# Kernel tuning notes

Hardware: AMD Instinct MI355X
Metric: run time of the kernel (lower is better)

Reference implementation:

```python
import jax, jax.numpy as jnp
import numpy as np

N = 100_000      # target ('paper') nodes
E_RAND = 500_000 # random metapath edges (self-loops added on top)
C = 256          # channels
H = 8            # heads
D = C // H       # proj_dim = 32
SEM = 128        # semantic attention hidden
NEG_SLOPE = 0.2


def _edges(k):
    e = jax.random.randint(k, (2, E_RAND), 0, N, dtype=jnp.int32)
    loops = jnp.broadcast_to(jnp.arange(N, dtype=jnp.int32), (2, N))
    return jnp.concatenate([e, loops], axis=1)  # [2, E_RAND + N]


def setup_inputs() -> dict:
    key = jax.random.key(0)
    ks = jax.random.split(key, 9)
    return {
        "x": jax.random.normal(ks[0], (N, C), dtype=jnp.float32),
        "W": jax.random.normal(ks[1], (D, C), dtype=jnp.float32) * (1.0 / np.sqrt(C)),
        "att1": jax.random.normal(ks[2], (H, 2 * D), dtype=jnp.float32) * (1.0 / np.sqrt(2 * D)),
        "att2": jax.random.normal(ks[3], (H, 2 * D), dtype=jnp.float32) * (1.0 / np.sqrt(2 * D)),
        "fc_w": jax.random.normal(ks[4], (SEM, C), dtype=jnp.float32) * (1.0 / np.sqrt(C)),
        "fc_b": jnp.zeros((SEM,), dtype=jnp.float32),
        "q": jax.random.normal(ks[5], (SEM,), dtype=jnp.float32) * (1.0 / np.sqrt(SEM)),
        "ei1": _edges(ks[6]),
        "ei2": _edges(ks[7]),
    }


def _segment_softmax(e, dst, num_nodes):
    # numerically stable softmax over edges grouped by destination node
    m = jax.ops.segment_max(e, dst, num_segments=num_nodes)      # [N, H]
    ex = jnp.exp(e - m[dst])                                     # [E, H]
    s = jax.ops.segment_sum(ex, dst, num_segments=num_nodes)     # [N, H]
    return ex / s[dst]


def _gat_layer(h, ei, att):
    # h: [N, d] projected target features; ei: [2, E]; att: [H, 2d]
    src, dst = ei[0], ei[1]
    n, d = h.shape
    a_dst, a_src = att[:, :d], att[:, d:]   # cat order in torch: [h_i(dst), h_j(src)]
    # per-edge attention logits [E, H] without materializing [E, H, 2d]
    e = jax.nn.leaky_relu(h[dst] @ a_dst.T + h[src] @ a_src.T, NEG_SLOPE)
    alpha = _segment_softmax(e, dst, n)                          # [E, H]
    m = h[src][:, None, :] * alpha[:, :, None]                   # [E, H, d]
    out = jax.ops.segment_sum(m, dst, num_segments=n)            # [N, H, d]
    return jax.nn.elu(out).reshape(n, H * d)                     # [N, H*d]


def reference(x, W, att1, att2, fc_w, fc_b, q, ei1, ei2):
    # type-specific projection (bias-free Linear): [N, C] -> [N, d]
    h = x @ W.T
    Z1 = _gat_layer(h, ei1, att1)
    Z2 = _gat_layer(h, ei2, att2)
    # semantic attention across meta-paths
    def score(Z):
        return (jnp.tanh(Z @ fc_w.T + fc_b) @ q).mean()
    V = jax.nn.softmax(jnp.stack([score(Z1), score(Z2)]))        # [2]
    return V[0] * Z1 + V[1] * Z2                                 # [N, C]
```

## Files before the change

kernel.cpp:

```cpp
#include <hip/hip_runtime.h>
#include <math.h>

#define Nn 100000
#define Cc 256
#define Dd 32
#define Hh 8
#define SEMk 128
#define PAD 32
#define NEG 0.2f
#define NB1 25000
#define NBS 1563

#if __has_builtin(__builtin_amdgcn_exp2f)
#define EXP2(x) __builtin_amdgcn_exp2f(x)
#else
#define EXP2(x) exp2f(x)
#endif
#define LOG2E 1.44269504088896f

typedef __attribute__((ext_vector_type(8))) short bf16x8;
typedef __attribute__((ext_vector_type(4))) short s16x4;
typedef __attribute__((ext_vector_type(4))) float f32x4;

__device__ __forceinline__ short f2bf(float f) {
    unsigned u = __float_as_uint(f);
    u = (u + 0x7FFF + ((u >> 16) & 1)) >> 16;
    return (short)u;
}

__global__ __launch_bounds__(256) void k_prep(const float* __restrict__ W,
                                              float* __restrict__ Wt,
                                              const float* __restrict__ fcw,
                                              short* __restrict__ fcwb) {
    int i = blockIdx.x * 256 + threadIdx.x;
    if (i < Dd * Cc) {
        int j = i >> 5, k = i & 31;
        Wt[i] = W[k * Cc + j];
    }
    if (i < SEMk * Cc) fcwb[i] = f2bf(fcw[i]);
}

__global__ __launch_bounds__(256) void k_hproj(const float* __restrict__ x,
                                               const float* __restrict__ Wt,
                                               const float* __restrict__ att1,
                                               const float* __restrict__ att2,
                                               float* __restrict__ h,
                                               float* __restrict__ sd1, float* __restrict__ ss1,
                                               float* __restrict__ sd2, float* __restrict__ ss2) {
    __shared__ float4 xs[32 * 65];
    __shared__ float  wt[256 * 36];
    __shared__ float4 hs[32 * 9];
    __shared__ float  a1[8 * 68];
    __shared__ float  a2[8 * 68];

    int t = threadIdx.x;
    int nb = blockIdx.x * 32;

    const float4* xg = (const float4*)x + (size_t)nb * 64;
#pragma unroll
    for (int it = 0; it < 8; ++it) {
        int i = t + it * 256;
        xs[(i >> 6) * 65 + (i & 63)] = xg[i];
    }
    const float4* wg = (const float4*)Wt;
#pragma unroll
    for (int it = 0; it < 8; ++it) {
        int i = t + it * 256;
        *(float4*)&wt[(i >> 3) * 36 + (i & 7) * 4] = wg[i];
    }
#pragma unroll
    for (int it = 0; it < 2; ++it) {
        int i = t + it * 256;
        a1[(i >> 6) * 68 + (i & 63)] = att1[i];
        a2[(i >> 6) * 68 + (i & 63)] = att2[i];
    }
    __syncthreads();

    int nl = t >> 3;
    int dq = t & 7;
    float4 acc = make_float4(0.f, 0.f, 0.f, 0.f);
    const float4* xr = &xs[nl * 65];
#pragma unroll 4
    for (int j4 = 0; j4 < 64; ++j4) {
        float4 xv = xr[j4];
        float4 w0 = *(const float4*)&wt[(j4 * 4 + 0) * 36 + dq * 4];
        float4 w1 = *(const float4*)&wt[(j4 * 4 + 1) * 36 + dq * 4];
        float4 w2 = *(const float4*)&wt[(j4 * 4 + 2) * 36 + dq * 4];
        float4 w3 = *(const float4*)&wt[(j4 * 4 + 3) * 36 + dq * 4];
        acc.x += xv.x * w0.x + xv.y * w1.x + xv.z * w2.x + xv.w * w3.x;
        acc.y += xv.x * w0.y + xv.y * w1.y + xv.z * w2.y + xv.w * w3.y;
        acc.z += xv.x * w0.z + xv.y * w1.z + xv.z * w2.z + xv.w * w3.z;
        acc.w += xv.x * w0.w + xv.y * w1.w + xv.z * w2.w + xv.w * w3.w;
    }
    ((float4*)h)[(size_t)(nb + nl) * 8 + dq] = acc;
    hs[nl * 9 + dq] = acc;
    __syncthreads();

    int nl2 = t >> 3;
    int hh = t & 7;
    float d1 = 0.f, s1 = 0.f, d2 = 0.f, s2 = 0.f;
#pragma unroll
    for (int d4 = 0; d4 < 8; ++d4) {
        float4 hv = hs[nl2 * 9 + d4];
        float4 ad1 = *(const float4*)&a1[hh * 68 + d4 * 4];
        float4 as1 = *(const float4*)&a1[hh * 68 + 32 + d4 * 4];
        float4 ad2 = *(const float4*)&a2[hh * 68 + d4 * 4];
        float4 as2 = *(const float4*)&a2[hh * 68 + 32 + d4 * 4];
        d1 += hv.x * ad1.x + hv.y * ad1.y + hv.z * ad1.z + hv.w * ad1.w;
        s1 += hv.x * as1.x + hv.y * as1.y + hv.z * as1.z + hv.w * as1.w;
        d2 += hv.x * ad2.x + hv.y * ad2.y + hv.z * ad2.z + hv.w * ad2.w;
        s2 += hv.x * as2.x + hv.y * as2.y + hv.z * as2.z + hv.w * as2.w;
    }
    int n = nb + nl2;
    sd1[n * 8 + hh] = d1 * LOG2E; ss1[n * 8 + hh] = s1 * LOG2E;
    sd2[n * 8 + hh] = d2 * LOG2E; ss2[n * 8 + hh] = s2 * LOG2E;
}

__global__ __launch_bounds__(256) void k_scatter(const int* __restrict__ ei1, int E1,
                                                 const int* __restrict__ ei2, int E2,
                                                 int* __restrict__ cnt,
                                                 int* __restrict__ slt1,
                                                 int* __restrict__ slt2) {
    int id = blockIdx.x * 256 + threadIdx.x;
    const int* ei; int e, EE; int* c; int* sl;
    if (id < E1) { ei = ei1; e = id; EE = E1; c = cnt; sl = slt1; }
    else {
        e = id - E1;
        if (e >= E2) return;
        ei = ei2; EE = E2; c = cnt + Nn; sl = slt2;
    }
    int s = ei[e];
    int d = ei[EE + e];
    int pos = atomicAdd(&c[d], 1);
    if (pos < PAD) sl[d * PAD + pos] = s;
}

#define LOADC(S0,S1,S2,S3,A0,A1,A2,A3,V0,V1,V2,V3,BB) do {                         \
    S0 = __shfl(sval, (BB) + 0); S1 = __shfl(sval, (BB) + 1);                      \
    S2 = __shfl(sval, (BB) + 2); S3 = __shfl(sval, (BB) + 3);                      \
    S1 = ((BB) + 1 < deg) ? S1 : n;                                                \
    S2 = ((BB) + 2 < deg) ? S2 : n;                                                \
    S3 = ((BB) + 3 < deg) ? S3 : n;                                                \
    A0 = ssrc[(unsigned)S0 * 8u + hh]; A1 = ssrc[(unsigned)S1 * 8u + hh];          \
    A2 = ssrc[(unsigned)S2 * 8u + hh]; A3 = ssrc[(unsigned)S3 * 8u + hh];          \
    V0 = h4[(unsigned)S0 * 8u + sub];  V1 = h4[(unsigned)S1 * 8u + sub];           \
    V2 = h4[(unsigned)S2 * 8u + sub];  V3 = h4[(unsigned)S3 * 8u + sub];           \
} while (0)

#define CONS(A0,A1,A2,A3,V0,V1,V2,V3,BB) do {                                      \
    float ev_, w_;                                                                 \
    ev_ = sd + A0; ev_ = ev_ > 0.f ? ev_ : NEG * ev_; w_ = EXP2(ev_);              \
    acc.x += w_ * V0.x; acc.y += w_ * V0.y; acc.z += w_ * V0.z; acc.w += w_ * V0.w; ssum += w_; \
    ev_ = sd + A1; ev_ = ev_ > 0.f ? ev_ : NEG * ev_; w_ = EXP2(ev_);              \
    w_ = ((BB) + 1 < deg) ? w_ : 0.f;                                              \
    acc.x += w_ * V1.x; acc.y += w_ * V1.y; acc.z += w_ * V1.z; acc.w += w_ * V1.w; ssum += w_; \
    ev_ = sd + A2; ev_ = ev_ > 0.f ? ev_ : NEG * ev_; w_ = EXP2(ev_);              \
    w_ = ((BB) + 2 < deg) ? w_ : 0.f;                                              \
    acc.x += w_ * V2.x; acc.y += w_ * V2.y; acc.z += w_ * V2.z; acc.w += w_ * V2.w; ssum += w_; \
    ev_ = sd + A3; ev_ = ev_ > 0.f ? ev_ : NEG * ev_; w_ = EXP2(ev_);              \
    w_ = ((BB) + 3 < deg) ? w_ : 0.f;                                              \
    acc.x += w_ * V3.x; acc.y += w_ * V3.y; acc.z += w_ * V3.z; acc.w += w_ * V3.w; ssum += w_; \
} while (0)

__global__ __launch_bounds__(256, 4) void k_gat(const float* __restrict__ h,
                                                const float* __restrict__ sd1, const float* __restrict__ ss1,
                                                const float* __restrict__ sd2, const float* __restrict__ ss2,
                                                const int* __restrict__ cnt,
                                                const int* __restrict__ slt1, const int* __restrict__ slt2,
                                                float* __restrict__ Z1, float* __restrict__ Z2) {
    int blk = blockIdx.x;
    const float* sdst = sd1; const float* ssrc = ss1;
    const int* cc = cnt; const int* sl = slt1; float* Z = Z1;
    if (blk >= NB1) { blk -= NB1; sdst = sd2; ssrc = ss2; cc = cnt + Nn; sl = slt2; Z = Z2; }
    int t = threadIdx.x;
    int lane = t & 63;
    int n = blk * 4 + (t >> 6);
    int deg = cc[n]; if (deg > PAD) deg = PAD;
    int hh = lane >> 3;
    int sub = lane & 7;
    float sd = sdst[n * 8 + hh];
    int sval = sl[n * PAD + (lane & 31)];
    const float4* h4 = (const float4*)h;

    float ssum = 0.f;
    float4 acc = make_float4(0.f, 0.f, 0.f, 0.f);

    int as0, as1, as2, as3;  float aa0, aa1, aa2, aa3;  float4 av0, av1, av2, av3;
    int bs0, bs1, bs2, bs3;  float ba0, ba1, ba2, ba3;  float4 bv0, bv1, bv2, bv3;

    LOADC(as0, as1, as2, as3, aa0, aa1, aa2, aa3, av0, av1, av2, av3, 0);
    int base = 0;
    for (;;) {
        int nxt = base + 4;
        bool more = nxt < deg;
        if (more) LOADC(bs0, bs1, bs2, bs3, ba0, ba1, ba2, ba3, bv0, bv1, bv2, bv3, nxt);
        CONS(aa0, aa1, aa2, aa3, av0, av1, av2, av3, base);
        if (!more) break;
        base = nxt;
        nxt = base + 4;
        more = nxt < deg;
        if (more) LOADC(as0, as1, as2, as3, aa0, aa1, aa2, aa3, av0, av1, av2, av3, nxt);
        CONS(ba0, ba1, ba2, ba3, bv0, bv1, bv2, bv3, base);
        if (!more) break;
        base = nxt;
    }

    float inv = 1.f / ssum;
    float4 o;
    o.x = acc.x * inv; o.y = acc.y * inv; o.z = acc.z * inv; o.w = acc.w * inv;
    o.x = o.x > 0.f ? o.x : __expf(o.x) - 1.f;
    o.y = o.y > 0.f ? o.y : __expf(o.y) - 1.f;
    o.z = o.z > 0.f ? o.z : __expf(o.z) - 1.f;
    o.w = o.w > 0.f ? o.w : __expf(o.w) - 1.f;
    ((float4*)Z)[(size_t)n * 64 + lane] = o;
}

__device__ __forceinline__ float fast_tanh(float x) {
    return 1.f - 2.f / (1.f + __expf(2.f * x));
}

__global__ __launch_bounds__(256) void k_score(const float* __restrict__ Z1,
                        const float* __restrict__ Z2,
                        const short* __restrict__ fcwb,
                        const float* __restrict__ fcb,
                        const float* __restrict__ q,
                        float* __restrict__ Sacc) {
    int blk = blockIdx.x;
    const float* Z = Z1; float* bins = Sacc;
    if (blk >= NBS) { blk -= NBS; Z = Z2; bins = Sacc + 256; }
    int t = threadIdx.x;
    int lane = t & 63;
    int wid = t >> 6;
    int nodebase = blk * 64 + wid * 16;
    if (nodebase >= Nn) return;
    int col = lane & 15;
    int quad = lane >> 4;

    const float* zp = Z + (size_t)(nodebase + col) * Cc + quad * 8;
    bf16x8 af[8];
#pragma unroll
    for (int ks = 0; ks < 8; ++ks) {
        float4 f0 = *(const float4*)(zp + ks * 32);
        float4 f1 = *(const float4*)(zp + ks * 32 + 4);
        bf16x8 a;
        a[0] = f2bf(f0.x); a[1] = f2bf(f0.y); a[2] = f2bf(f0.z); a[3] = f2bf(f0.w);
        a[4] = f2bf(f1.x); a[5] = f2bf(f1.y); a[6] = f2bf(f1.z); a[7] = f2bf(f1.w);
        af[ks] = a;
    }

    f32x4 acc[8];
#pragma unroll
    for (int tt = 0; tt < 8; ++tt) { acc[tt][0] = 0.f; acc[tt][1] = 0.f; acc[tt][2] = 0.f; acc[tt][3] = 0.f; }

    const short* brow = fcwb + (size_t)col * Cc + quad * 8;
#pragma unroll
    for (int ks = 0; ks < 8; ++ks) {
#pragma unroll
        for (int tt = 0; tt < 8; ++tt) {
            bf16x8 b = *(const bf16x8*)(brow + tt * 4096 + ks * 32);
            acc[tt] = __builtin_amdgcn_mfma_f32_16x16x32_bf16(af[ks], b, acc[tt], 0, 0, 0);
        }
    }

    float local = 0.f;
#pragma unroll
    for (int tt = 0; tt < 8; ++tt) {
        int sem = tt * 16 + col;
        float b = fcb[sem], qq = q[sem];
#pragma unroll
        for (int r = 0; r < 4; ++r) local += fast_tanh(acc[tt][r] + b) * qq;
    }
#pragma unroll
    for (int off = 32; off > 0; off >>= 1) local += __shfl_down(local, off);
    if (lane == 0) atomicAdd(&bins[(blk & 15) * 16], local);
}

__global__ __launch_bounds__(256) void k_combine(float* __restrict__ out,
                                                 const float* __restrict__ Z2,
                                                 const float* __restrict__ S) {
    float s1 = 0.f, s2 = 0.f;
#pragma unroll
    for (int i = 0; i < 16; ++i) { s1 += S[i * 16]; s2 += S[256 + i * 16]; }
    s1 *= (1.f / (float)Nn);
    s2 *= (1.f / (float)Nn);
    float mx = fmaxf(s1, s2);
    float e1 = __expf(s1 - mx), e2 = __expf(s2 - mx);
    float inv = 1.f / (e1 + e2);
    float V0 = e1 * inv, V1 = e2 * inv;
    size_t i = (size_t)blockIdx.x * 256 + threadIdx.x;
    if (i < (size_t)Nn * 64) {
        float4 a = ((float4*)out)[i];
        float4 b = ((const float4*)Z2)[i];
        a.x = V0 * a.x + V1 * b.x;
        a.y = V0 * a.y + V1 * b.y;
        a.z = V0 * a.z + V1 * b.z;
        a.w = V0 * a.w + V1 * b.w;
        ((float4*)out)[i] = a;
    }
}

extern "C" void kernel_launch(void* const* d_in, const int* in_sizes, int n_in,
                              void* d_out, int out_size, void* d_ws, size_t ws_size,
                              hipStream_t stream) {
    const float* x    = (const float*)d_in[0];
    const float* W    = (const float*)d_in[1];
    const float* att1 = (const float*)d_in[2];
    const float* att2 = (const float*)d_in[3];
    const float* fcw  = (const float*)d_in[4];
    const float* fcb  = (const float*)d_in[5];
    const float* q    = (const float*)d_in[6];
    const int*   ei1  = (const int*)d_in[7];
    const int*   ei2  = (const int*)d_in[8];
    int E1 = in_sizes[7] / 2;
    int E2 = in_sizes[8] / 2;
    float* out = (float*)d_out;

    char* ws = (char*)d_ws;
    size_t off = 0;
    auto alloc = [&](size_t bytes) -> char* {
        char* p = ws + off;
        off = (off + bytes + 255) & ~(size_t)255;
        return p;
    };
    float* Z2   = (float*)alloc((size_t)Nn * Cc * 4);
    float* h    = (float*)alloc((size_t)Nn * Dd * 4);
    float* sd1  = (float*)alloc((size_t)Nn * Hh * 4);
    float* ss1  = (float*)alloc((size_t)Nn * Hh * 4);
    float* sd2  = (float*)alloc((size_t)Nn * Hh * 4);
    float* ss2  = (float*)alloc((size_t)Nn * Hh * 4);
    int*   cnt  = (int*)alloc((size_t)2 * Nn * 4);
    float* red  = (float*)alloc(2048);
    float* Wt   = (float*)alloc((size_t)Dd * Cc * 4);
    short* fcwb = (short*)alloc((size_t)SEMk * Cc * 2);
    int*   slt1 = (int*)alloc((size_t)Nn * PAD * 4);
    int*   slt2 = (int*)alloc((size_t)Nn * PAD * 4);
    (void)ws_size; (void)n_in; (void)out_size;

    hipMemsetAsync(cnt, 0, (size_t)2 * Nn * 4, stream);
    hipMemsetAsync(red, 0, 2048, stream);

    k_prep<<<(SEMk * Cc + 255) / 256, 256, 0, stream>>>(W, Wt, fcw, fcwb);
    k_hproj<<<Nn / 32, 256, 0, stream>>>(x, Wt, att1, att2, h, sd1, ss1, sd2, ss2);
    k_scatter<<<(E1 + E2 + 255) / 256, 256, 0, stream>>>(ei1, E1, ei2, E2, cnt, slt1, slt2);
    k_gat<<<2 * NB1, 256, 0, stream>>>(h, sd1, ss1, sd2, ss2, cnt, slt1, slt2, out, Z2);
    k_score<<<2 * NBS, 256, 0, stream>>>(out, Z2, fcwb, fcb, q, red);
    k_combine<<<(Nn * 64) / 256, 256, 0, stream>>>(out, Z2, red);
}
```

Before: 543.4 us.

## Fuse semantic-attention scoring into GAT aggregation kernel via shared-memory bf16 tile

The separate score kernel is merged into the GAT kernel. Each 1024-thread block now aggregates 16 nodes, converts the outputs to bf16 in LDS, and then 8 waves each run one 16-column MFMA slice of the fc projection, followed by tanh·q and an atomic add. This removes the re-read of Z1/Z2 from global memory and one kernel launch. In exchange it adds a block-wide barrier, leaves half the waves idle during the scoring phase, and the larger blocks may lower occupancy for the latency-bound gather.

Result: no change. 542.5 us (-0.2%).

```diff
diff --git a/kernel.cpp b/kernel.cpp
--- a/kernel.cpp
+++ b/kernel.cpp
@@ -8,8 +8,7 @@
 #define SEMk 128
 #define PAD 32
 #define NEG 0.2f
-#define NB1 25000
-#define NBS 1563
+#define NBF 6250
 
 #if __has_builtin(__builtin_amdgcn_exp2f)
 #define EXP2(x) __builtin_amdgcn_exp2f(x)
@@ -162,19 +161,26 @@
     acc.x += w_ * V3.x; acc.y += w_ * V3.y; acc.z += w_ * V3.z; acc.w += w_ * V3.w; ssum += w_; \
 } while (0)
 
-__global__ __launch_bounds__(256, 4) void k_gat(const float* __restrict__ h,
-                                                const float* __restrict__ sd1, const float* __restrict__ ss1,
-                                                const float* __restrict__ sd2, const float* __restrict__ ss2,
-                                                const int* __restrict__ cnt,
-                                                const int* __restrict__ slt1, const int* __restrict__ slt2,
-                                                float* __restrict__ Z1, float* __restrict__ Z2) {
+__global__ __launch_bounds__(1024, 8) void k_gatsc(const float* __restrict__ h,
+                                                   const float* __restrict__ sd1, const float* __restrict__ ss1,
+                                                   const float* __restrict__ sd2, const float* __restrict__ ss2,
+                                                   const int* __restrict__ cnt,
+                                                   const int* __restrict__ slt1, const int* __restrict__ slt2,
+                                                   float* __restrict__ Z1, float* __restrict__ Z2,
+                                                   const short* __restrict__ fcwb,
+                                                   const float* __restrict__ fcb,
+                                                   const float* __restrict__ q,
+                                                   float* __restrict__ Sacc) {
+    __shared__ short zls[16 * 264];
     int blk = blockIdx.x;
     const float* sdst = sd1; const float* ssrc = ss1;
     const int* cc = cnt; const int* sl = slt1; float* Z = Z1;
-    if (blk >= NB1) { blk -= NB1; sdst = sd2; ssrc = ss2; cc = cnt + Nn; sl = slt2; Z = Z2; }
+    float* bins = Sacc;
+    if (blk >= NBF) { blk -= NBF; sdst = sd2; ssrc = ss2; cc = cnt + Nn; sl = slt2; Z = Z2; bins = Sacc + 256; }
     int t = threadIdx.x;
     int lane = t & 63;
-    int n = blk * 4 + (t >> 6);
+    int wid = t >> 6;
+    int n = blk * 16 + wid;
     int deg = cc[n]; if (deg > PAD) deg = PAD;
     int hh = lane >> 3;
     int sub = lane & 7;
@@ -213,66 +219,36 @@
     o.z = o.z > 0.f ? o.z : __expf(o.z) - 1.f;
     o.w = o.w > 0.f ? o.w : __expf(o.w) - 1.f;
     ((float4*)Z)[(size_t)n * 64 + lane] = o;
-}
-
-__device__ __forceinline__ float fast_tanh(float x) {
-    return 1.f - 2.f / (1.f + __expf(2.f * x));
-}
-
-__global__ __launch_bounds__(256) void k_score(const float* __restrict__ Z1,
-                        const float* __restrict__ Z2,
-                        const short* __restrict__ fcwb,
-                        const float* __restrict__ fcb,
-                        const float* __restrict__ q,
-                        float* __restrict__ Sacc) {
-    int blk = blockIdx.x;
-    const float* Z = Z1; float* bins = Sacc;
-    if (blk >= NBS) { blk -= NBS; Z = Z2; bins = Sacc + 256; }
-    int t = threadIdx.x;
-    int lane = t & 63;
-    int wid = t >> 6;
-    int nodebase = blk * 64 + wid * 16;
-    if (nodebase >= Nn) return;
+
+    s16x4 b4;
+    b4[0] = f2bf(o.x); b4[1] = f2bf(o.y); b4[2] = f2bf(o.z); b4[3] = f2bf(o.w);
+    *(s16x4*)&zls[wid * 264 + lane * 4] = b4;
+    __syncthreads();
+
+    if (wid >= 8) return;
+
     int col = lane & 15;
     int quad = lane >> 4;
-
-    const float* zp = Z + (size_t)(nodebase + col) * Cc + quad * 8;
-    bf16x8 af[8];
+    const short* zrow = &zls[col * 264 + quad * 8];
+    const short* brow = fcwb + (size_t)(wid * 16 + col) * Cc + quad * 8;
+    f32x4 sacc;
+    sacc[0] = 0.f; sacc[1] = 0.f; sacc[2] = 0.f; sacc[3] = 0.f;
 #pragma unroll
     for (int ks = 0; ks < 8; ++ks) {
-        float4 f0 = *(const float4*)(zp + ks * 32);
-        float4 f1 = *(const float4*)(zp + ks * 32 + 4);
-        bf16x8 a;
-        a[0] = f2bf(f0.x); a[1] = f2bf(f0.y); a[2] = f2bf(f0.z); a[3] = f2bf(f0.w);
-        a[4] = f2bf(f1.x); a[5] = f2bf(f1.y); a[6] = f2bf(f1.z); a[7] = f2bf(f1.w);
-        af[ks] = a;
-    }
-
-    f32x4 acc[8];
-#pragma unroll
-    for (int tt = 0; tt < 8; ++tt) { acc[tt][0] = 0.f; acc[tt][1] = 0.f; acc[tt][2] = 0.f; acc[tt][3] = 0.f; }
-
-    const short* brow = fcwb + (size_t)col * Cc + quad * 8;
-#pragma unroll
-    for (int ks = 0; ks < 8; ++ks) {
-#pragma unroll
-        for (int tt = 0; tt < 8; ++tt) {
-            bf16x8 b = *(const bf16x8*)(brow + tt * 4096 + ks * 32);
-            acc[tt] = __builtin_amdgcn_mfma_f32_16x16x32_bf16(af[ks], b, acc[tt], 0, 0, 0);
-        }
-    }
-
+        bf16x8 a = *(const bf16x8*)(zrow + ks * 32);
+        bf16x8 b = *(const bf16x8*)(brow + ks * 32);
+        sacc = __builtin_amdgcn_mfma_f32_16x16x32_bf16(a, b, sacc, 0, 0, 0);
+    }
     float local = 0.f;
-#pragma unroll
-    for (int tt = 0; tt < 8; ++tt) {
-        int sem = tt * 16 + col;
-        float b = fcb[sem], qq = q[sem];
-#pragma unroll
-        for (int r = 0; r < 4; ++r) local += fast_tanh(acc[tt][r] + b) * qq;
+    {
+        int sem = wid * 16 + col;
+        float bb = fcb[sem], qq = q[sem];
+#pragma unroll
+        for (int r = 0; r < 4; ++r) local += (1.f - 2.f / (1.f + __expf(2.f * (sacc[r] + bb)))) * qq;
     }
 #pragma unroll
     for (int off = 32; off > 0; off >>= 1) local += __shfl_down(local, off);
-    if (lane == 0) atomicAdd(&bins[(blk & 15) * 16], local);
+    if (lane == 0) atomicAdd(&bins[(blk & 31) * 8], local);
 }
 
 __global__ __launch_bounds__(256) void k_combine(float* __restrict__ out,
@@ -280,7 +256,7 @@
                                                  const float* __restrict__ S) {
     float s1 = 0.f, s2 = 0.f;
 #pragma unroll
-    for (int i = 0; i < 16; ++i) { s1 += S[i * 16]; s2 += S[256 + i * 16]; }
+    for (int i = 0; i < 32; ++i) { s1 += S[i * 8]; s2 += S[256 + i * 8]; }
     s1 *= (1.f / (float)Nn);
     s2 *= (1.f / (float)Nn);
     float mx = fmaxf(s1, s2);
@@ -342,7 +318,7 @@
     k_prep<<<(SEMk * Cc + 255) / 256, 256, 0, stream>>>(W, Wt, fcw, fcwb);
     k_hproj<<<Nn / 32, 256, 0, stream>>>(x, Wt, att1, att2, h, sd1, ss1, sd2, ss2);
     k_scatter<<<(E1 + E2 + 255) / 256, 256, 0, stream>>>(ei1, E1, ei2, E2, cnt, slt1, slt2);
-    k_gat<<<2 * NB1, 256, 0, stream>>>(h, sd1, ss1, sd2, ss2, cnt, slt1, slt2, out, Z2);
-    k_score<<<2 * NBS, 256, 0, stream>>>(out, Z2, fcwb, fcb, q, red);
+    k_gatsc<<<2 * NBF, 1024, 0, stream>>>(h, sd1, ss1, sd2, ss2, cnt, slt1, slt2,
+                                          out, Z2, fcwb, fcb, q, red);
     k_combine<<<(Nn * 64) / 256, 256, 0, stream>>>(out, Z2, red);
 }
```

## Stage score-kernel Z tiles through LDS with coalesced swizzled direct loads

Applied to the files above, without the earlier changes.

The semantic score kernel now loads each wave's 16x256 Z tile into shared memory with global_load_lds in coalesced 1KB row chunks, using an XOR swizzle to avoid bank conflicts. Fragments are then read from LDS instead of through strided per-lane global loads. Each wave handles one 16-node task, and the B-operand loads are batched ahead of the MFMAs. The atomic bins are spread over 32 slots. The cost is 64KB of LDS per block, which limits occupancy.

Result: faster. 528.8 us (-2.7%).

```diff
diff --git a/kernel.cpp b/kernel.cpp
--- a/kernel.cpp
+++ b/kernel.cpp
@@ -9,7 +9,7 @@
 #define PAD 32
 #define NEG 0.2f
 #define NB1 25000
-#define NBS 1563
+#define NTASK 12500
 
 #if __has_builtin(__builtin_amdgcn_exp2f)
 #define EXP2(x) __builtin_amdgcn_exp2f(x)
@@ -219,29 +219,47 @@
     return 1.f - 2.f / (1.f + __expf(2.f * x));
 }
 
+#define SWZ(off, r) ((off) ^ (((r) & 7) << 4))
+
 __global__ __launch_bounds__(256) void k_score(const float* __restrict__ Z1,
                         const float* __restrict__ Z2,
                         const short* __restrict__ fcwb,
                         const float* __restrict__ fcb,
                         const float* __restrict__ q,
                         float* __restrict__ Sacc) {
-    int blk = blockIdx.x;
-    const float* Z = Z1; float* bins = Sacc;
-    if (blk >= NBS) { blk -= NBS; Z = Z2; bins = Sacc + 256; }
+    __shared__ float zst[4 * 4096];
     int t = threadIdx.x;
     int lane = t & 63;
     int wid = t >> 6;
-    int nodebase = blk * 64 + wid * 16;
-    if (nodebase >= Nn) return;
+    int task = blockIdx.x * 4 + wid;
+    const float* Z = Z1; float* bins = Sacc;
+    int tile = task;
+    if (task >= NTASK / 2) { Z = Z2; bins = Sacc + 256; tile = task - NTASK / 2; }
+    int nodebase = tile * 16;
+    float* myst = &zst[wid * 4096];
+
+    const char* zb = (const char*)(Z + (size_t)nodebase * Cc);
+#pragma unroll
+    for (int r = 0; r < 16; ++r) {
+        const char* src = zb + r * 1024 + SWZ(lane * 16, r);
+        __builtin_amdgcn_global_load_lds(
+            (const __attribute__((address_space(1))) void*)src,
+            (__attribute__((address_space(3))) void*)(myst + r * 256),
+            16, 0, 0);
+    }
+    asm volatile("s_waitcnt vmcnt(0)" ::: "memory");
+    __builtin_amdgcn_sched_barrier(0);
+
     int col = lane & 15;
     int quad = lane >> 4;
 
-    const float* zp = Z + (size_t)(nodebase + col) * Cc + quad * 8;
+    const char* rowp = (const char*)myst + col * 1024;
     bf16x8 af[8];
 #pragma unroll
     for (int ks = 0; ks < 8; ++ks) {
-        float4 f0 = *(const float4*)(zp + ks * 32);
-        float4 f1 = *(const float4*)(zp + ks * 32 + 4);
+        int b0 = ks * 128 + quad * 32;
+        float4 f0 = *(const float4*)(rowp + SWZ(b0, col));
+        float4 f1 = *(const float4*)(rowp + SWZ(b0 + 16, col));
         bf16x8 a;
         a[0] = f2bf(f0.x); a[1] = f2bf(f0.y); a[2] = f2bf(f0.z); a[3] = f2bf(f0.w);
         a[4] = f2bf(f1.x); a[5] = f2bf(f1.y); a[6] = f2bf(f1.z); a[7] = f2bf(f1.w);
@@ -255,11 +273,13 @@
     const short* brow = fcwb + (size_t)col * Cc + quad * 8;
 #pragma unroll
     for (int ks = 0; ks < 8; ++ks) {
-#pragma unroll
-        for (int tt = 0; tt < 8; ++tt) {
-            bf16x8 b = *(const bf16x8*)(brow + tt * 4096 + ks * 32);
-            acc[tt] = __builtin_amdgcn_mfma_f32_16x16x32_bf16(af[ks], b, acc[tt], 0, 0, 0);
-        }
+        bf16x8 bf[8];
+#pragma unroll
+        for (int tt = 0; tt < 8; ++tt)
+            bf[tt] = *(const bf16x8*)(brow + tt * 4096 + ks * 32);
+#pragma unroll
+        for (int tt = 0; tt < 8; ++tt)
+            acc[tt] = __builtin_amdgcn_mfma_f32_16x16x32_bf16(af[ks], bf[tt], acc[tt], 0, 0, 0);
     }
 
     float local = 0.f;
@@ -272,7 +292,7 @@
     }
 #pragma unroll
     for (int off = 32; off > 0; off >>= 1) local += __shfl_down(local, off);
-    if (lane == 0) atomicAdd(&bins[(blk & 15) * 16], local);
+    if (lane == 0) atomicAdd(&bins[(task & 31) * 8], local);
 }
 
 __global__ __launch_bounds__(256) void k_combine(float* __restrict__ out,
@@ -280,7 +300,7 @@
                                                  const float* __restrict__ S) {
     float s1 = 0.f, s2 = 0.f;
 #pragma unroll
-    for (int i = 0; i < 16; ++i) { s1 += S[i * 16]; s2 += S[256 + i * 16]; }
+    for (int i = 0; i < 32; ++i) { s1 += S[i * 8]; s2 += S[256 + i * 8]; }
     s1 *= (1.f / (float)Nn);
     s2 *= (1.f / (float)Nn);
     float mx = fmaxf(s1, s2);
@@ -343,6 +363,6 @@
     k_hproj<<<Nn / 32, 256, 0, stream>>>(x, Wt, att1, att2, h, sd1, ss1, sd2, ss2);
     k_scatter<<<(E1 + E2 + 255) / 256, 256, 0, stream>>>(ei1, E1, ei2, E2, cnt, slt1, slt2);
     k_gat<<<2 * NB1, 256, 0, stream>>>(h, sd1, ss1, sd2, ss2, cnt, slt1, slt2, out, Z2);
-    k_score<<<2 * NBS, 256, 0, stream>>>(out, Z2, fcwb, fcb, q, red);
+    k_score<<<NTASK / 4, 256, 0, stream>>>(out, Z2, fcwb, fcb, q, red);
     k_combine<<<(Nn * 64) / 256, 256, 0, stream>>>(out, Z2, red);
 }
```
